# Kernel tuning notes

Hardware: AMD Instinct MI355X
Metric: run time of the kernel (lower is better)

The kernel has to match this reference:

```python
import jax, jax.numpy as jnp
import numpy as np

# dims: batch, seq, model dim, heads, head_k_dim, head_v_dim, conv size
B, S, D, H, DK, DV, K = 1, 2048, 1024, 8, 128, 128, 4
KD, VD = H * DK, H * DV  # key_dim, value_dim


def _silu(x):
    return x * jax.nn.sigmoid(x)


def _l2norm(x, eps=1e-6):
    return x * jax.lax.rsqrt(jnp.sum(x * x, -1, keepdims=True) + eps)


def _causal_conv_silu(x, w):
    # depthwise causal conv1d (ShortConvolution, activation='silu', no bias)
    # x: [b, s, d], w: [d, K]
    Kc = w.shape[1]
    xp = jnp.pad(x, ((0, 0), (Kc - 1, 0), (0, 0)))
    y = sum(xp[:, i:i + x.shape[1], :] * w[:, i] for i in range(Kc))
    return _silu(y)


def _rmsnorm(x, w, eps=1e-5):
    return x * jax.lax.rsqrt(jnp.mean(x * x, -1, keepdims=True) + eps) * w


def _kda(q, k, v, g, beta):
    # gated delta-rule linear attention (KDA), recurrent form == chunk_kda math
    # q,k,g: [B,S,H,DK]; v: [B,S,H,DV]; beta: [B,S,H]
    scale = DK ** -0.5
    qn = _l2norm(q) * scale  # use_qk_l2norm_in_kernel=True
    kn = _l2norm(k)

    def step(Sm, inp):
        q_t, k_t, v_t, g_t, b_t = inp  # [B,H,DK], [B,H,DK], [B,H,DV], [B,H,DK], [B,H]
        Sm = Sm * jnp.exp(g_t)[..., None]                    # per-key-channel decay
        v_new = (v_t - jnp.einsum('bhk,bhkv->bhv', k_t, Sm)) * b_t[..., None]
        Sm = Sm + k_t[..., None] * v_new[..., None, :]       # delta-rule update
        o_t = jnp.einsum('bhk,bhkv->bhv', q_t, Sm)
        return Sm, o_t

    xs = (jnp.swapaxes(qn, 0, 1), jnp.swapaxes(kn, 0, 1), jnp.swapaxes(v, 0, 1),
          jnp.swapaxes(g, 0, 1), jnp.swapaxes(beta, 0, 1))
    S0 = jnp.zeros((q.shape[0], H, DK, DV), jnp.float32)
    _, o = jax.lax.scan(step, S0, xs)
    return jnp.swapaxes(o, 0, 1)  # [B,S,H,DV]


def setup_inputs() -> dict:
    key = jax.random.key(0)
    ks = jax.random.split(key, 20)

    def w(k, shape, fan_in):
        return jax.random.normal(k, shape, jnp.float32) / np.sqrt(fan_in)

    return {
        'x': jax.random.normal(ks[0], (B, S, D), jnp.float32),
        've': jax.random.normal(ks[1], (B, S, D), jnp.float32),
        'sa_lambdas': jax.random.uniform(ks[2], (2,), jnp.float32),
        'Wq': w(ks[3], (KD, D), D), 'Wk': w(ks[4], (KD, D), D), 'Wv': w(ks[5], (VD, D), D),
        'Wo': w(ks[6], (D, VD), VD),
        'wq_conv': w(ks[7], (KD, K), K), 'wk_conv': w(ks[8], (KD, K), K), 'wv_conv': w(ks[9], (VD, K), K),
        'Wf1': w(ks[10], (DV, D), D), 'Wf2': w(ks[11], (KD, DV), DV),
        'Wb': w(ks[12], (H, D), D),
        'A_log': jnp.log(jax.random.uniform(ks[13], (H,), jnp.float32, 1.0, 16.0)),
        'dt_bias': jnp.zeros((KD,), jnp.float32),
        'Wg1': w(ks[14], (DV, D), D), 'Wg2': w(ks[15], (VD, DV), DV),
        'bg2': jnp.zeros((VD,), jnp.float32),
        'w_norm': jnp.ones((DV,), jnp.float32),
    }


def reference(x, ve, sa_lambdas, Wq, Wk, Wv, Wo, wq_conv, wk_conv, wv_conv,
              Wf1, Wf2, Wb, A_log, dt_bias, Wg1, Wg2, bg2, w_norm):
    b, s, _ = x.shape
    # q/k/v projections + short causal conv with silu
    q = _causal_conv_silu(x @ Wq.T, wq_conv)
    k = _causal_conv_silu(x @ Wk.T, wk_conv)
    v = _causal_conv_silu(x @ Wv.T, wv_conv)
    # fused_kda_gate: g = -exp(A_log) * softplus(f_proj(x) + dt_bias), per [H, DK]
    g = (x @ Wf1.T) @ Wf2.T
    g = jax.nn.softplus((g + dt_bias).astype(jnp.float32)).reshape(b, s, H, DK)
    g = -jnp.exp(A_log)[None, None, :, None] * g
    beta = jax.nn.sigmoid((x @ Wb.T).astype(jnp.float32))  # [b,s,H]
    q = q.reshape(b, s, H, DK)
    k = k.reshape(b, s, H, DK)
    v = v.reshape(b, s, H, DV)
    # mix v with value-embedding ve (3-D branch of _mix_v_with_ve)
    ve_v = _causal_conv_silu(ve @ Wv.T, wv_conv).reshape(b, s, H, DV)
    v = sa_lambdas[0] * v + sa_lambdas[1] * ve_v
    o = _kda(q, k, v, g, beta)  # [b,s,H,DV]
    # FusedRMSNormGated(activation='sigmoid'): rmsnorm(o)*w then gate
    g_out = ((x @ Wg1.T) @ Wg2.T + bg2).reshape(b, s, H, DV)
    o = _rmsnorm(o, w_norm) * jax.nn.sigmoid(g_out)
    return o.reshape(b, s, VD) @ Wo.T
```

## Files before the change

kernel.cpp:

```cpp
#include <hip/hip_runtime.h>
#include <math.h>
#include <stdint.h>

#define S_LEN 2048
#define DMODEL 1024
#define NH 8
#define DK_ 128
#define DV_ 128
#define KD_ 1024
#define KCONV 4
#define CW 32
#define NW2 64
#define PREB_STRIDE 17408
#define TKH_OFF 0
#define QHT_OFF 4096
#define KCT_OFF 8192
#define TV_OFF 12288
#define NN_OFF 16384
#define RS 164
#define GS 20

typedef short bf16x8 __attribute__((ext_vector_type(8)));
typedef float f32x4 __attribute__((ext_vector_type(4)));

__device__ __forceinline__ uint16_t f2bf(float f) {
  uint32_t u = __float_as_uint(f);
  u += 0x7FFF + ((u >> 16) & 1);
  return (uint16_t)(u >> 16);
}
__device__ __forceinline__ float bf2f(uint16_t u) {
  return __uint_as_float((uint32_t)u << 16);
}
__device__ __forceinline__ void glds16(const uint16_t* g, uint16_t* l) {
  __builtin_amdgcn_global_load_lds(
      (const __attribute__((address_space(1))) void*)g,
      (__attribute__((address_space(3))) void*)l, 16, 0, 0);
}
__device__ __forceinline__ float dot4(float4 a, float4 b) {
  return fmaf(a.w, b.w, fmaf(a.z, b.z, fmaf(a.y, b.y, a.x * b.x)));
}
__device__ __forceinline__ float4 f4add(float4 a, float4 b) {
  float4 r; r.x = a.x + b.x; r.y = a.y + b.y; r.z = a.z + b.z; r.w = a.w + b.w; return r;
}
__device__ __forceinline__ float4 f4sub(float4 a, float4 b) {
  float4 r; r.x = a.x - b.x; r.y = a.y - b.y; r.z = a.z - b.z; r.w = a.w - b.w; return r;
}
__device__ __forceinline__ float4 f4mul(float4 a, float4 b) {
  float4 r; r.x = a.x * b.x; r.y = a.y * b.y; r.z = a.z * b.z; r.w = a.w * b.w; return r;
}
__device__ __forceinline__ float4 f4s(float4 a, float s) {
  float4 r; r.x = a.x * s; r.y = a.y * s; r.z = a.z * s; r.w = a.w * s; return r;
}
__device__ __forceinline__ float4 f4expc(float4 a) {
  float4 r;
  r.x = expf(fminf(a.x, 0.f)); r.y = expf(fminf(a.y, 0.f));
  r.z = expf(fminf(a.z, 0.f)); r.w = expf(fminf(a.w, 0.f));
  return r;
}
__device__ __forceinline__ float4 f4exp(float4 a) {
  float4 r; r.x = expf(a.x); r.y = expf(a.y); r.z = expf(a.z); r.w = expf(a.w); return r;
}
__device__ __forceinline__ uint4 pack8(float4 a, float4 b) {
  uint4 r;
  r.x = (uint32_t)f2bf(a.x) | ((uint32_t)f2bf(a.y) << 16);
  r.y = (uint32_t)f2bf(a.z) | ((uint32_t)f2bf(a.w) << 16);
  r.z = (uint32_t)f2bf(b.x) | ((uint32_t)f2bf(b.y) << 16);
  r.w = (uint32_t)f2bf(b.z) | ((uint32_t)f2bf(b.w) << 16);
  return r;
}
__device__ __forceinline__ uint2 pack4(f32x4 a) {
  uint2 r;
  r.x = (uint32_t)f2bf(a[0]) | ((uint32_t)f2bf(a[1]) << 16);
  r.y = (uint32_t)f2bf(a[2]) | ((uint32_t)f2bf(a[3]) << 16);
  return r;
}
union U4B8 { uint4 u; bf16x8 b; };
__device__ __forceinline__ bf16x8 u2b(uint4 u) { U4B8 x; x.u = u; return x.b; }

#define DPPADD(x, ctrl) \
  x += __int_as_float(__builtin_amdgcn_update_dpp(0, __float_as_int(x), ctrl, 0xF, 0xF, true))

__device__ __forceinline__ void row8_sum2(float& a, float& b) {
  DPPADD(a, 0xB1); DPPADD(b, 0xB1);
  DPPADD(a, 0x4E); DPPADD(b, 0x4E);
  DPPADD(a, 0x141); DPPADD(b, 0x141);
}
__device__ __forceinline__ void row8_arr8x2(float* x, float* y) {
#pragma unroll
  for (int i = 0; i < 8; i++) { DPPADD(x[i], 0xB1); DPPADD(y[i], 0xB1); }
#pragma unroll
  for (int i = 0; i < 8; i++) { DPPADD(x[i], 0x4E); DPPADD(y[i], 0x4E); }
#pragma unroll
  for (int i = 0; i < 8; i++) { DPPADD(x[i], 0x141); DPPADD(y[i], 0x141); }
}

struct CastArgs {
  const float* s[8];
  uint16_t* d[8];
  int n[8];
};
__global__ __launch_bounds__(256) void cast_multi(CastArgs a, const float* __restrict__ Wb,
                                                  uint16_t* __restrict__ Wbp) {
  int i = blockIdx.y;
  if (i == 8) {
    for (int idx = blockIdx.x * 256 + threadIdx.x; idx < 128 * 1024; idx += 256 * 256) {
      int r = idx >> 10;
      Wbp[idx] = (r < 8) ? f2bf(Wb[idx]) : (uint16_t)0;
    }
    return;
  }
  const int step = gridDim.x * 256 * 8;
  for (int base = (blockIdx.x * 256 + threadIdx.x) * 8; base < a.n[i]; base += step) {
    const float4* sp = (const float4*)(a.s[i] + base);
    float4 x0 = sp[0], x1 = sp[1];
    *(uint4*)(a.d[i] + base) = pack8(x0, x1);
  }
}

__global__ __launch_bounds__(256) void gemm_wc(
    const float* __restrict__ A,
    const float* __restrict__ B,
    uint16_t* __restrict__ C) {
  __shared__ float As[16][68];
  __shared__ float Bs[16][68];
  const int tid = threadIdx.x;
  const int m0 = blockIdx.y * 64, n0 = blockIdx.x * 64;
  const int tx = tid & 15, ty = tid >> 4;
  const int lk = tid & 15, lr = tid >> 4;
  const int bc = tid & 63, bkr = tid >> 6;
  float acc[4][4] = {};
  for (int k0 = 0; k0 < 128; k0 += 16) {
#pragma unroll
    for (int i = 0; i < 4; i++) {
      As[lk][lr + 16 * i] = A[(size_t)(m0 + lr + 16 * i) * 128 + k0 + lk];
      Bs[bkr + 4 * i][bc] = B[(size_t)(k0 + bkr + 4 * i) * 1024 + n0 + bc];
    }
    __syncthreads();
#pragma unroll
    for (int kk = 0; kk < 16; kk++) {
      float4 a4 = *(const float4*)&As[kk][ty * 4];
      float4 b4 = *(const float4*)&Bs[kk][tx * 4];
      float av[4] = {a4.x, a4.y, a4.z, a4.w};
      float bv[4] = {b4.x, b4.y, b4.z, b4.w};
#pragma unroll
      for (int i = 0; i < 4; i++)
#pragma unroll
        for (int jx = 0; jx < 4; jx++) acc[i][jx] = fmaf(av[i], bv[jx], acc[i][jx]);
    }
    __syncthreads();
  }
#pragma unroll
  for (int i = 0; i < 4; i++)
#pragma unroll
    for (int jx = 0; jx < 4; jx++)
      C[(size_t)(m0 + ty * 4 + i) * 1024 + n0 + tx * 4 + jx] = f2bf(acc[i][jx]);
}

__device__ __forceinline__ void gemm_body(
    const uint16_t* __restrict__ A, const uint16_t* __restrict__ B, void* C,
    int N, int K, int outbf, int bx, int by, int tid,
    uint16_t* Asb, uint16_t* Bsb) {
  const int n0 = bx * 128;
  if (n0 >= N) return;
  const int w = tid >> 6, lane = tid & 63;
  const int m0 = by * 128;
  const int mw = (w & 1) * 64, nw = (w >> 1) * 64;
  const int c0 = tid, c1 = 256 + tid;
  const int r0 = c0 >> 2, cl0 = (c0 & 3) ^ ((r0 >> 2) & 3);
  const int r1 = c1 >> 2, cl1 = (c1 & 3) ^ ((r1 >> 2) & 3);
  const uint16_t* gA0 = A + (size_t)(m0 + r0) * K + cl0 * 8;
  const uint16_t* gA1 = A + (size_t)(m0 + r1) * K + cl1 * 8;
  const uint16_t* gB0 = B + (size_t)(n0 + r0) * K + cl0 * 8;
  const uint16_t* gB1 = B + (size_t)(n0 + r1) * K + cl1 * 8;
  uint16_t* lA0 = Asb + w * 512;
  uint16_t* lA1 = Asb + 2048 + w * 512;
  uint16_t* lB0 = Bsb + w * 512;
  uint16_t* lB1 = Bsb + 2048 + w * 512;

  const int l15 = lane & 15, q = lane >> 4;
  const int ccq = q ^ ((l15 >> 2) & 3);

  f32x4 acc[4][4] = {};
  for (int k0 = 0; k0 < K; k0 += 32) {
    glds16(gA0 + k0, lA0);
    glds16(gA1 + k0, lA1);
    glds16(gB0 + k0, lB0);
    glds16(gB1 + k0, lB1);
    __syncthreads();
    bf16x8 af[4], bfr[4];
#pragma unroll
    for (int i = 0; i < 4; i++)
      af[i] = *(const bf16x8*)&Asb[(mw + i * 16 + l15) * 32 + ccq * 8];
#pragma unroll
    for (int jx = 0; jx < 4; jx++)
      bfr[jx] = *(const bf16x8*)&Bsb[(nw + jx * 16 + l15) * 32 + ccq * 8];
#pragma unroll
    for (int i = 0; i < 4; i++)
#pragma unroll
      for (int jx = 0; jx < 4; jx++)
        acc[i][jx] = __builtin_amdgcn_mfma_f32_16x16x32_bf16(af[i], bfr[jx],
                                                             acc[i][jx], 0, 0, 0);
    __syncthreads();
  }
#pragma unroll
  for (int i = 0; i < 4; i++) {
#pragma unroll
    for (int jx = 0; jx < 4; jx++) {
      int n = n0 + nw + jx * 16 + l15;
#pragma unroll
      for (int r = 0; r < 4; r++) {
        int m = m0 + mw + i * 16 + q * 4 + r;
        if (outbf)
          ((uint16_t*)C)[(size_t)m * N + n] = f2bf(acc[i][jx][r]);
        else
          ((float*)C)[(size_t)m * N + n] = acc[i][jx][r];
      }
    }
  }
}

struct GJobs {
  const uint16_t* A[8];
  const uint16_t* B[8];
  void* C[8];
  int N[8];
  int outbf[8];
};
__global__ __launch_bounds__(256) void gemm_mfma(GJobs j, int K) {
  __shared__ uint16_t Asb[128 * 32];
  __shared__ uint16_t Bsb[128 * 32];
  const int z = blockIdx.z;
  gemm_body(j.A[z], j.B[z], j.C[z], j.N[z], K, j.outbf[z],
            blockIdx.x, blockIdx.y, threadIdx.x, Asb, Bsb);
}

__global__ __launch_bounds__(256) void conv_silu_mix(
    const uint16_t* __restrict__ qp, const uint16_t* __restrict__ kp,
    const uint16_t* __restrict__ vp, const uint16_t* __restrict__ vep,
    const float* __restrict__ wq, const float* __restrict__ wk,
    const float* __restrict__ wv, const float* __restrict__ lam,
    float* __restrict__ qc, float* __restrict__ kc, float* __restrict__ vmx) {
  int idx = blockIdx.x * 256 + threadIdx.x;
  if (idx >= S_LEN * KD_ / 8) return;
  int s = idx >> 7;
  int d0 = (idx & 127) * 8;
  const float lam0 = lam[0], lam1 = lam[1];

  union { uint4 u; ushort h[8]; } t;
  size_t base = (size_t)s * KD_ + d0;

  {
    float4 w4[8];
#pragma unroll
    for (int c = 0; c < 8; c++) w4[c] = *(const float4*)(wq + (size_t)d0 * 4 + c * 4);
    float acc[8] = {};
#pragma unroll
    for (int i = 0; i < KCONV; i++) {
      int ss = s - (KCONV - 1) + i;
      if (ss < 0) continue;
      t.u = *(const uint4*)(qp + (size_t)ss * KD_ + d0);
#pragma unroll
      for (int c = 0; c < 8; c++)
        acc[c] = fmaf(bf2f(t.h[c]), ((const float*)&w4[c])[i], acc[c]);
    }
    float out[8];
#pragma unroll
    for (int c = 0; c < 8; c++) out[c] = acc[c] / (1.f + expf(-acc[c]));
    *(float4*)(qc + base) = *(float4*)&out[0];
    *(float4*)(qc + base + 4) = *(float4*)&out[4];
  }
  {
    float4 w4[8];
#pragma unroll
    for (int c = 0; c < 8; c++) w4[c] = *(const float4*)(wk + (size_t)d0 * 4 + c * 4);
    float acc[8] = {};
#pragma unroll
    for (int i = 0; i < KCONV; i++) {
      int ss = s - (KCONV - 1) + i;
      if (ss < 0) continue;
      t.u = *(const uint4*)(kp + (size_t)ss * KD_ + d0);
#pragma unroll
      for (int c = 0; c < 8; c++)
        acc[c] = fmaf(bf2f(t.h[c]), ((const float*)&w4[c])[i], acc[c]);
    }
    float out[8];
#pragma unroll
    for (int c = 0; c < 8; c++) out[c] = acc[c] / (1.f + expf(-acc[c]));
    *(float4*)(kc + base) = *(float4*)&out[0];
    *(float4*)(kc + base + 4) = *(float4*)&out[4];
  }
  {
    float4 w4[8];
#pragma unroll
    for (int c = 0; c < 8; c++) w4[c] = *(const float4*)(wv + (size_t)d0 * 4 + c * 4);
    float av[8] = {}, ae[8] = {};
#pragma unroll
    for (int i = 0; i < KCONV; i++) {
      int ss = s - (KCONV - 1) + i;
      if (ss < 0) continue;
      size_t off = (size_t)ss * KD_ + d0;
      t.u = *(const uint4*)(vp + off);
#pragma unroll
      for (int c = 0; c < 8; c++)
        av[c] = fmaf(bf2f(t.h[c]), ((const float*)&w4[c])[i], av[c]);
      t.u = *(const uint4*)(vep + off);
#pragma unroll
      for (int c = 0; c < 8; c++)
        ae[c] = fmaf(bf2f(t.h[c]), ((const float*)&w4[c])[i], ae[c]);
    }
    float out[8];
#pragma unroll
    for (int c = 0; c < 8; c++) {
      float sv = av[c] / (1.f + expf(-av[c]));
      float se = ae[c] / (1.f + expf(-ae[c]));
      out[c] = lam0 * sv + lam1 * se;
    }
    *(float4*)(vmx + base) = *(float4*)&out[0];
    *(float4*)(vmx + base + 4) = *(float4*)&out[4];
  }
}

__global__ __launch_bounds__(256) void kda_pre(
    const float* __restrict__ qc, const float* __restrict__ kc,
    const float* __restrict__ graw, const float* __restrict__ vm,
    const float* __restrict__ bpre, const float* __restrict__ dt_bias,
    const float* __restrict__ A_log, uint16_t* __restrict__ preB,
    float* __restrict__ preF) {
  __shared__ float kls[32 * RS];
  __shared__ float Gls[32 * RS];
  __shared__ float Mcm[32 * 36];
  __shared__ float bls[32];
  const int w = blockIdx.x >> 3, h = blockIdx.x & 7;
  const int tid = threadIdx.x;
  const int t = tid >> 3, kq = tid & 7;
  const int wv = tid >> 6;
  const size_t gb = (size_t)blockIdx.x * PREB_STRIDE;
  const size_t gf = (size_t)blockIdx.x * 128;

  size_t roff = (size_t)(w * CW + t) * KD_ + h * DK_ + kq * 16;
  float4 kv[4], qv[4], gv[4], dtb[4];
#pragma unroll
  for (int i = 0; i < 4; i++) {
    kv[i] = *(const float4*)(kc + roff + i * 4);
    qv[i] = *(const float4*)(qc + roff + i * 4);
    gv[i] = *(const float4*)(graw + roff + i * 4);
    dtb[i] = *(const float4*)(dt_bias + h * DK_ + kq * 16 + i * 4);
  }
  const float Ahead = expf(A_log[h]);
  if (tid < 32) {
    float b = bpre[(size_t)(w * CW + tid) * 128 + h];
    bls[tid] = 1.f / (1.f + expf(-b));
  }
  float src[32];
  if (tid >= 128) {
    int c2 = tid - 128;
#pragma unroll
    for (int t2 = 0; t2 < 32; t2++)
      src[t2] = vm[(size_t)(w * CW + t2) * KD_ + h * DV_ + c2];
  }
#pragma unroll
  for (int i = 0; i < 4; i++) {
    float vsp[4];
    float xin[4] = {gv[i].x + dtb[i].x, gv[i].y + dtb[i].y,
                    gv[i].z + dtb[i].z, gv[i].w + dtb[i].w};
#pragma unroll
    for (int e = 0; e < 4; e++)
      vsp[e] = (xin[e] > 20.f) ? xin[e] : log1pf(expf(xin[e]));
    gv[i].x = -Ahead * vsp[0]; gv[i].y = -Ahead * vsp[1];
    gv[i].z = -Ahead * vsp[2]; gv[i].w = -Ahead * vsp[3];
  }
  float sk = 0.f, sq = 0.f;
#pragma unroll
  for (int i = 0; i < 4; i++) {
    sk += dot4(kv[i], kv[i]);
    sq += dot4(qv[i], qv[i]);
  }
  row8_sum2(sk, sq);
  float rkn = rsqrtf(sk + 1e-6f);
  float rqn = rsqrtf(sq + 1e-6f) * 0.08838834764831845f;
#pragma unroll
  for (int i = 0; i < 4; i++) {
    kv[i] = f4s(kv[i], rkn);
    qv[i] = f4s(qv[i], rqn);
    *(float4*)&kls[t * RS + kq * GS + i * 4] = kv[i];
    *(float4*)&Gls[t * RS + kq * GS + i * 4] = gv[i];
  }
  __syncthreads();
  float4 Ga[4] = {};
#pragma unroll
  for (int jb = 0; jb < 4; jb++) {
    if (jb <= wv) {
#pragma unroll
      for (int jj = 0; jj < 8; jj++) {
        int j = jb * 8 + jj;
        bool inc = (jb < wv) || (j <= t);
#pragma unroll
        for (int i = 0; i < 4; i++) {
          float4 gj = *(const float4*)&Gls[j * RS + kq * GS + i * 4];
          if (inc) Ga[i] = f4add(Ga[i], gj);
        }
      }
    }
  }
  __syncthreads();
  float4 khr[4];
  float4 Pa[4];
#pragma unroll
  for (int i = 0; i < 4; i++) {
    *(float4*)&Gls[t * RS + kq * GS + i * 4] = Ga[i];
    Pa[i] = f4exp(Ga[i]);
    khr[i] = f4mul(kv[i], Pa[i]);
  }
  {
    float4 q0 = f4mul(qv[0], Pa[0]), q1 = f4mul(qv[1], Pa[1]);
    float4 q2 = f4mul(qv[2], Pa[2]), q3 = f4mul(qv[3], Pa[3]);
    *(uint4*)(preB + gb + QHT_OFF + t * 128 + kq * 16) = pack8(q0, q1);
    *(uint4*)(preB + gb + QHT_OFF + t * 128 + kq * 16 + 8) = pack8(q2, q3);
  }
  if (t == 31) {
#pragma unroll
    for (int i = 0; i < 4; i++)
      *(float4*)(preF + gf + kq * 16 + i * 4) = Pa[i];
  }
  __syncthreads();
#pragma unroll
  for (int i = 0; i < 4; i++) {
    float4 Gfi = *(const float4*)&Gls[31 * RS + kq * GS + i * 4];
    float4 ea = f4expc(f4sub(Gfi, Ga[i]));
    float4 kc4 = f4mul(kv[i], ea);
    float kk[4] = {kc4.x, kc4.y, kc4.z, kc4.w};
#pragma unroll
    for (int e = 0; e < 4; e++)
      preB[gb + KCT_OFF + (kq * 16 + i * 4 + e) * 32 + t] = f2bf(kk[e]);
  }
#pragma unroll
  for (int jb = 0; jb < 4; jb++) {
    if (jb <= wv) {
      float mp8[8], np8[8];
#pragma unroll
      for (int jj = 0; jj < 8; jj++) {
        int j = jb * 8 + jj;
        float m = 0.f, n = 0.f;
#pragma unroll
        for (int i = 0; i < 4; i++) {
          float4 kj = *(const float4*)&kls[j * RS + kq * GS + i * 4];
          float4 Gj = *(const float4*)&Gls[j * RS + kq * GS + i * 4];
          float4 e = f4expc(f4sub(Ga[i], Gj));
          float4 p = f4mul(kj, e);
          m += dot4(kv[i], p);
          n += dot4(qv[i], p);
        }
        mp8[jj] = (j < t) ? m : 0.f;
        np8[jj] = (j <= t) ? n : 0.f;
      }
      row8_arr8x2(mp8, np8);
#pragma unroll
      for (int jj = 0; jj < 8; jj++) {
        if (kq == jj) {
          int j = jb * 8 + jj;
          Mcm[j * 36 + t] = bls[t] * mp8[jj];
          preB[gb + NN_OFF + t * 32 + j] = f2bf(np8[jj]);
        }
      }
    } else {
      preB[gb + NN_OFF + t * 32 + jb * 8 + kq] = 0;
    }
  }
  float bl[32];
#pragma unroll
  for (int i = 0; i < 8; i++) {
    float4 b4 = *(const float4*)&bls[i * 4];
    bl[i * 4 + 0] = b4.x; bl[i * 4 + 1] = b4.y;
    bl[i * 4 + 2] = b4.z; bl[i * 4 + 3] = b4.w;
  }
  __syncthreads();
#pragma unroll
  for (int i = 0; i < 4; i++)
    *(float4*)&kls[t * RS + kq * GS + i * 4] = khr[i];
  __syncthreads();
  if (tid < 128) {
#pragma unroll
    for (int t2 = 0; t2 < 32; t2++)
      src[t2] = kls[t2 * RS + (tid >> 4) * GS + (tid & 15)];
  }
  const int c = tid;
  float acc[32];
#pragma unroll
  for (int i = 0; i < 32; i++) acc[i] = 0.f;
#pragma unroll
  for (int t2 = 0; t2 < 32; t2++) {
    float val = fmaf(bl[t2], src[t2], -acc[t2]);
    if (c < 128)
      preB[gb + TKH_OFF + t2 * 128 + c] = f2bf(val);
    else
      preB[gb + TV_OFF + t2 * 128 + (c - 128)] = f2bf(val);
#pragma unroll
    for (int t3 = t2 + 1; t3 < 32; t3++)
      acc[t3] = fmaf(Mcm[t2 * 36 + t3], val, acc[t3]);
  }
}

__global__ __launch_bounds__(256) void kda_scan_g2(
    const uint16_t* __restrict__ preB, const float* __restrict__ preF,
    float* __restrict__ o, const uint16_t* __restrict__ g1b,
    const uint16_t* __restrict__ Wg2b, float* __restrict__ g2raw) {
  __shared__ uint16_t tkh[2][32 * 136];
  __shared__ uint16_t qht[2][32 * 136];
  __shared__ uint16_t sbf[16 * 136];
  __shared__ uint16_t vbf[16 * 40];
  __shared__ uint16_t Asb[128 * 32];
  __shared__ uint16_t Bsb[128 * 32];
  const int bid = blockIdx.x;
  const int tid = threadIdx.x;

  if (bid >= 64) {
    int b2 = bid - 64;
    gemm_body(g1b, Wg2b, g2raw, 1024, 128, 0, b2 & 7, b2 >> 3, tid, Asb, Bsb);
    return;
  }

  const int h = bid & 7, cg = bid >> 3;
  const int wv = tid >> 6, lane = tid & 63;
  const int q = lane >> 4, l15 = lane & 15;

  auto stage = [&](int w, int buf) {
    size_t gbs = (size_t)(w * 8 + h) * PREB_STRIDE;
    const uint4* gt = (const uint4*)(preB + gbs + TKH_OFF);
    const uint4* gq = (const uint4*)(preB + gbs + QHT_OFF);
    int row = lane >> 1, half = lane & 1;
    uint4 a[8], b[8];
#pragma unroll
    for (int i = 0; i < 8; i++) {
      a[i] = gt[lane * 8 + i];
      b[i] = gq[lane * 8 + i];
    }
#pragma unroll
    for (int i = 0; i < 8; i++) {
      *(uint4*)&tkh[buf][row * 136 + half * 64 + i * 8] = a[i];
      *(uint4*)&qht[buf][row * 136 + half * 64 + i * 8] = b[i];
    }
  };

  f32x4 s[8] = {};

  if (wv == 1) stage(0, 0);
  __syncthreads();

  for (int w = 0; w < NW2; w++) {
    if (wv == 1) {
      if (w + 1 < NW2) stage(w + 1, (w + 1) & 1);
    } else if (wv == 0) {
      const int buf = w & 1;
      const size_t gbs = (size_t)(w * 8 + h) * PREB_STRIDE;
      uint4 kct[8], nrg[2];
      float4 pb[8];
      float tvv[2][4];
#pragma unroll
      for (int ki = 0; ki < 8; ki++)
        kct[ki] = *(const uint4*)(preB + gbs + KCT_OFF + (16 * ki + l15) * 32 + q * 8);
#pragma unroll
      for (int tt = 0; tt < 2; tt++)
        nrg[tt] = *(const uint4*)(preB + gbs + NN_OFF + (tt * 16 + l15) * 32 + q * 8);
#pragma unroll
      for (int ki = 0; ki < 8; ki++)
        pb[ki] = *(const float4*)(preF + (size_t)(w * 8 + h) * 128 + 16 * ki + q * 4);
#pragma unroll
      for (int tt = 0; tt < 2; tt++)
#pragma unroll
        for (int r = 0; r < 4; r++)
          tvv[tt][r] = bf2f(preB[gbs + TV_OFF + (tt * 16 + q * 4 + r) * 128 + cg * 16 + l15]);
#pragma unroll
      for (int ki = 0; ki < 8; ki++)
        *(uint2*)&sbf[l15 * 136 + 16 * ki + q * 4] = pack4(s[ki]);
      f32x4 aat[2] = {}, bbt[2] = {};
      __builtin_amdgcn_s_setprio(1);
#pragma unroll
      for (int kc = 0; kc < 4; kc++) {
        bf16x8 bS = *(const bf16x8*)&sbf[l15 * 136 + kc * 32 + q * 8];
#pragma unroll
        for (int tt = 0; tt < 2; tt++) {
          bf16x8 aT = *(const bf16x8*)&tkh[buf][(tt * 16 + l15) * 136 + kc * 32 + q * 8];
          bf16x8 aQ = *(const bf16x8*)&qht[buf][(tt * 16 + l15) * 136 + kc * 32 + q * 8];
          aat[tt] = __builtin_amdgcn_mfma_f32_16x16x32_bf16(aT, bS, aat[tt], 0, 0, 0);
          bbt[tt] = __builtin_amdgcn_mfma_f32_16x16x32_bf16(aQ, bS, bbt[tt], 0, 0, 0);
        }
      }
      __builtin_amdgcn_s_setprio(0);
#pragma unroll
      for (int tt = 0; tt < 2; tt++) {
        f32x4 vn;
#pragma unroll
        for (int r = 0; r < 4; r++) vn[r] = tvv[tt][r] - aat[tt][r];
        *(uint2*)&vbf[l15 * 40 + tt * 16 + q * 4] = pack4(vn);
      }
      bf16x8 bV = *(const bf16x8*)&vbf[l15 * 40 + q * 8];
      __builtin_amdgcn_s_setprio(1);
#pragma unroll
      for (int tt = 0; tt < 2; tt++) {
        f32x4 ot = __builtin_amdgcn_mfma_f32_16x16x32_bf16(u2b(nrg[tt]), bV,
                                                           bbt[tt], 0, 0, 0);
#pragma unroll
        for (int r = 0; r < 4; r++)
          o[(size_t)(w * CW + tt * 16 + q * 4 + r) * KD_ + h * DK_ + cg * 16 + l15] = ot[r];
      }
#pragma unroll
      for (int ki = 0; ki < 8; ki++) {
#pragma unroll
        for (int r = 0; r < 4; r++) s[ki][r] *= pb[ki][r];
        s[ki] = __builtin_amdgcn_mfma_f32_16x16x32_bf16(u2b(kct[ki]), bV, s[ki], 0, 0, 0);
      }
      __builtin_amdgcn_s_setprio(0);
    }
    __syncthreads();
  }
}

__global__ __launch_bounds__(64) void gated_rmsnorm(
    const float* __restrict__ o, const float* __restrict__ g2raw,
    const float* __restrict__ bg2, const float* __restrict__ wn,
    uint16_t* __restrict__ ob) {
  size_t base = (size_t)blockIdx.x * DV_;
  int t = threadIdx.x;
  float a = o[base + t], b = o[base + t + 64];
  float ss = a * a + b * b;
#pragma unroll
  for (int off = 32; off > 0; off >>= 1) ss += __shfl_xor(ss, off);
  float r = rsqrtf(ss * (1.f / 128.f) + 1e-5f);
  int c0 = (int)((base + t) & 1023), c1 = (int)((base + t + 64) & 1023);
  float ga = 1.f / (1.f + expf(-(g2raw[base + t] + bg2[c0])));
  float gb = 1.f / (1.f + expf(-(g2raw[base + t + 64] + bg2[c1])));
  ob[base + t] = f2bf(a * r * wn[t] * ga);
  ob[base + t + 64] = f2bf(b * r * wn[t + 64] * gb);
}

extern "C" void kernel_launch(void* const* d_in, const int* in_sizes, int n_in,
                              void* d_out, int out_size, void* d_ws, size_t ws_size,
                              hipStream_t stream) {
  const float* x = (const float*)d_in[0];
  const float* ve = (const float*)d_in[1];
  const float* lam = (const float*)d_in[2];
  const float* Wq = (const float*)d_in[3];
  const float* Wk = (const float*)d_in[4];
  const float* Wv = (const float*)d_in[5];
  const float* Wo = (const float*)d_in[6];
  const float* wq_conv = (const float*)d_in[7];
  const float* wk_conv = (const float*)d_in[8];
  const float* wv_conv = (const float*)d_in[9];
  const float* Wf1 = (const float*)d_in[10];
  const float* Wf2 = (const float*)d_in[11];
  const float* Wb = (const float*)d_in[12];
  const float* A_log = (const float*)d_in[13];
  const float* dt_bias = (const float*)d_in[14];
  const float* Wg1 = (const float*)d_in[15];
  const float* Wg2 = (const float*)d_in[16];
  const float* bg2 = (const float*)d_in[17];
  const float* w_norm = (const float*)d_in[18];
  float* out = (float*)d_out;

  float* ws = (float*)d_ws;
  const size_t SZ = (size_t)S_LEN * KD_;
  uint16_t* qpb = (uint16_t*)ws;
  uint16_t* kpb = (uint16_t*)(ws + SZ / 2);
  uint16_t* vpb = (uint16_t*)(ws + SZ);
  uint16_t* vepb = (uint16_t*)(ws + 3 * SZ / 2);
  float* q_c = ws + 2 * SZ;
  float* k_c = ws + 3 * SZ;
  float* v_mix = ws + 4 * SZ;
  float* graw = ws + 5 * SZ;
  float* o_buf = graw;
  float* g2raw = k_c;
  uint16_t* bws = (uint16_t*)(ws + 6 * SZ);
  uint16_t* xb = bws;
  uint16_t* veb = xb + SZ;
  uint16_t* Wqb = veb + SZ;
  uint16_t* Wkb = Wqb + (size_t)KD_ * DMODEL;
  uint16_t* Wvb = Wkb + (size_t)KD_ * DMODEL;
  uint16_t* Wob = Wvb + (size_t)KD_ * DMODEL;
  uint16_t* Wg1b = Wob + (size_t)DMODEL * KD_;
  uint16_t* Wg2b = Wg1b + (size_t)DV_ * DMODEL;
  uint16_t* Wcb = Wg2b + (size_t)KD_ * DV_;
  uint16_t* Wbp = Wcb + (size_t)KD_ * DMODEL;
  uint16_t* g1b = Wbp + (size_t)128 * 1024;
  uint16_t* ob = g1b + (size_t)S_LEN * DV_;
  float* bpre2 = ws + 18 * (size_t)1024 * 1024;
  float* preF = ws + (size_t)20 * 1024 * 1024;
  uint16_t* preB = (uint16_t*)(ws + (size_t)20 * 1024 * 1024 + 65536 + 64);

  dim3 blk(256);

  CastArgs ca;
  ca.s[0] = x;   ca.d[0] = xb;   ca.n[0] = S_LEN * DMODEL;
  ca.s[1] = ve;  ca.d[1] = veb;  ca.n[1] = S_LEN * DMODEL;
  ca.s[2] = Wq;  ca.d[2] = Wqb;  ca.n[2] = KD_ * DMODEL;
  ca.s[3] = Wk;  ca.d[3] = Wkb;  ca.n[3] = KD_ * DMODEL;
  ca.s[4] = Wv;  ca.d[4] = Wvb;  ca.n[4] = KD_ * DMODEL;
  ca.s[5] = Wo;  ca.d[5] = Wob;  ca.n[5] = DMODEL * KD_;
  ca.s[6] = Wg1; ca.d[6] = Wg1b; ca.n[6] = DV_ * DMODEL;
  ca.s[7] = Wg2; ca.d[7] = Wg2b; ca.n[7] = KD_ * DV_;
  cast_multi<<<dim3(256, 9), blk, 0, stream>>>(ca, Wb, Wbp);

  gemm_wc<<<dim3(16, 16), blk, 0, stream>>>(Wf2, Wf1, Wcb);

  GJobs jq;
  jq.A[0] = xb;  jq.B[0] = Wqb;  jq.C[0] = qpb;   jq.N[0] = KD_; jq.outbf[0] = 1;
  jq.A[1] = xb;  jq.B[1] = Wkb;  jq.C[1] = kpb;   jq.N[1] = KD_; jq.outbf[1] = 1;
  jq.A[2] = xb;  jq.B[2] = Wvb;  jq.C[2] = vpb;   jq.N[2] = KD_; jq.outbf[2] = 1;
  jq.A[3] = veb; jq.B[3] = Wvb;  jq.C[3] = vepb;  jq.N[3] = KD_; jq.outbf[3] = 1;
  jq.A[4] = xb;  jq.B[4] = Wg1b; jq.C[4] = g1b;   jq.N[4] = DV_; jq.outbf[4] = 1;
  jq.A[5] = xb;  jq.B[5] = Wcb;  jq.C[5] = graw;  jq.N[5] = KD_; jq.outbf[5] = 0;
  jq.A[6] = xb;  jq.B[6] = Wbp;  jq.C[6] = bpre2; jq.N[6] = 128; jq.outbf[6] = 0;
  gemm_mfma<<<dim3(8, 16, 7), blk, 0, stream>>>(jq, DMODEL);

  int conv_blocks = (S_LEN * KD_ / 8 + 255) / 256;
  conv_silu_mix<<<conv_blocks, blk, 0, stream>>>(qpb, kpb, vpb, vepb,
                                                 wq_conv, wk_conv, wv_conv, lam,
                                                 q_c, k_c, v_mix);

  kda_pre<<<dim3(NW2 * 8), blk, 0, stream>>>(q_c, k_c, graw, v_mix, bpre2,
                                             dt_bias, A_log, preB, preF);

  kda_scan_g2<<<dim3(192), blk, 0, stream>>>(preB, preF, o_buf, g1b, Wg2b, g2raw);

  gated_rmsnorm<<<dim3(S_LEN * NH), dim3(64), 0, stream>>>(o_buf, g2raw, bg2,
                                                           w_norm, ob);

  GJobs jo;
  jo.A[0] = ob; jo.B[0] = Wob; jo.C[0] = out; jo.N[0] = DMODEL; jo.outbf[0] = 0;
  gemm_mfma<<<dim3(8, 16, 1), blk, 0, stream>>>(jo, KD_);
}
```

Measured before the change: 383.3 us.

## Fold Wf2·Wf1 weight GEMM into cast kernel and drop setprio hints

Moves the small fp32 GEMM that forms the combined Wf2·Wf1 weight into the multi-cast kernel as an extra grid row (blockIdx.y==9), so one launch does both jobs and the GEMM runs alongside the casts. This removes a kernel launch and the serialization between the two preprocessing kernels. It also removes the s_setprio wave-priority hints around the MFMA sections of the recurrent KDA kernel, which changes how waves are scheduled in the hot loop. The fused kernel now always allocates static LDS for the GEMM tiles, which may lower occupancy for the cast blocks.

After: 383.1 us. Within noise of the previous version (-0.0%).

```diff
diff --git a/kernel.cpp b/kernel.cpp
--- a/kernel.cpp
+++ b/kernel.cpp
@@ -99,9 +99,48 @@
   uint16_t* d[8];
   int n[8];
 };
-__global__ __launch_bounds__(256) void cast_multi(CastArgs a, const float* __restrict__ Wb,
-                                                  uint16_t* __restrict__ Wbp) {
+__global__ __launch_bounds__(256) void cast_multi(
+    CastArgs a, const float* __restrict__ Wb, uint16_t* __restrict__ Wbp,
+    const float* __restrict__ Wf2,
+    const float* __restrict__ Wf1,
+    uint16_t* __restrict__ Wcb) {
+  __shared__ float As[16][68];
+  __shared__ float Bs[16][68];
   int i = blockIdx.y;
+  if (i == 9) {
+    const int tid = threadIdx.x;
+    const int m0 = (blockIdx.x >> 4) * 64, n0 = (blockIdx.x & 15) * 64;
+    const int tx = tid & 15, ty = tid >> 4;
+    const int lk = tid & 15, lr = tid >> 4;
+    const int bc = tid & 63, bkr = tid >> 6;
+    float acc[4][4] = {};
+    for (int k0 = 0; k0 < 128; k0 += 16) {
+#pragma unroll
+      for (int ii = 0; ii < 4; ii++) {
+        As[lk][lr + 16 * ii] = Wf2[(size_t)(m0 + lr + 16 * ii) * 128 + k0 + lk];
+        Bs[bkr + 4 * ii][bc] = Wf1[(size_t)(k0 + bkr + 4 * ii) * 1024 + n0 + bc];
+      }
+      __syncthreads();
+#pragma unroll
+      for (int kk = 0; kk < 16; kk++) {
+        float4 a4 = *(const float4*)&As[kk][ty * 4];
+        float4 b4 = *(const float4*)&Bs[kk][tx * 4];
+        float av[4] = {a4.x, a4.y, a4.z, a4.w};
+        float bv[4] = {b4.x, b4.y, b4.z, b4.w};
+#pragma unroll
+        for (int ii = 0; ii < 4; ii++)
+#pragma unroll
+          for (int jx = 0; jx < 4; jx++) acc[ii][jx] = fmaf(av[ii], bv[jx], acc[ii][jx]);
+      }
+      __syncthreads();
+    }
+#pragma unroll
+    for (int ii = 0; ii < 4; ii++)
+#pragma unroll
+      for (int jx = 0; jx < 4; jx++)
+        Wcb[(size_t)(m0 + ty * 4 + ii) * 1024 + n0 + tx * 4 + jx] = f2bf(acc[ii][jx]);
+    return;
+  }
   if (i == 8) {
     for (int idx = blockIdx.x * 256 + threadIdx.x; idx < 128 * 1024; idx += 256 * 256) {
       int r = idx >> 10;
@@ -115,45 +154,6 @@
     float4 x0 = sp[0], x1 = sp[1];
     *(uint4*)(a.d[i] + base) = pack8(x0, x1);
   }
-}
-
-__global__ __launch_bounds__(256) void gemm_wc(
-    const float* __restrict__ A,
-    const float* __restrict__ B,
-    uint16_t* __restrict__ C) {
-  __shared__ float As[16][68];
-  __shared__ float Bs[16][68];
-  const int tid = threadIdx.x;
-  const int m0 = blockIdx.y * 64, n0 = blockIdx.x * 64;
-  const int tx = tid & 15, ty = tid >> 4;
-  const int lk = tid & 15, lr = tid >> 4;
-  const int bc = tid & 63, bkr = tid >> 6;
-  float acc[4][4] = {};
-  for (int k0 = 0; k0 < 128; k0 += 16) {
-#pragma unroll
-    for (int i = 0; i < 4; i++) {
-      As[lk][lr + 16 * i] = A[(size_t)(m0 + lr + 16 * i) * 128 + k0 + lk];
-      Bs[bkr + 4 * i][bc] = B[(size_t)(k0 + bkr + 4 * i) * 1024 + n0 + bc];
-    }
-    __syncthreads();
-#pragma unroll
-    for (int kk = 0; kk < 16; kk++) {
-      float4 a4 = *(const float4*)&As[kk][ty * 4];
-      float4 b4 = *(const float4*)&Bs[kk][tx * 4];
-      float av[4] = {a4.x, a4.y, a4.z, a4.w};
-      float bv[4] = {b4.x, b4.y, b4.z, b4.w};
-#pragma unroll
-      for (int i = 0; i < 4; i++)
-#pragma unroll
-        for (int jx = 0; jx < 4; jx++) acc[i][jx] = fmaf(av[i], bv[jx], acc[i][jx]);
-    }
-    __syncthreads();
-  }
-#pragma unroll
-  for (int i = 0; i < 4; i++)
-#pragma unroll
-    for (int jx = 0; jx < 4; jx++)
-      C[(size_t)(m0 + ty * 4 + i) * 1024 + n0 + tx * 4 + jx] = f2bf(acc[i][jx]);
 }
 
 __device__ __forceinline__ void gemm_body(
@@ -573,7 +573,6 @@
       for (int ki = 0; ki < 8; ki++)
         *(uint2*)&sbf[l15 * 136 + 16 * ki + q * 4] = pack4(s[ki]);
       f32x4 aat[2] = {}, bbt[2] = {};
-      __builtin_amdgcn_s_setprio(1);
 #pragma unroll
       for (int kc = 0; kc < 4; kc++) {
         bf16x8 bS = *(const bf16x8*)&sbf[l15 * 136 + kc * 32 + q * 8];
@@ -585,7 +584,6 @@
           bbt[tt] = __builtin_amdgcn_mfma_f32_16x16x32_bf16(aQ, bS, bbt[tt], 0, 0, 0);
         }
       }
-      __builtin_amdgcn_s_setprio(0);
 #pragma unroll
       for (int tt = 0; tt < 2; tt++) {
         f32x4 vn;
@@ -594,7 +592,6 @@
         *(uint2*)&vbf[l15 * 40 + tt * 16 + q * 4] = pack4(vn);
       }
       bf16x8 bV = *(const bf16x8*)&vbf[l15 * 40 + q * 8];
-      __builtin_amdgcn_s_setprio(1);
 #pragma unroll
       for (int tt = 0; tt < 2; tt++) {
         f32x4 ot = __builtin_amdgcn_mfma_f32_16x16x32_bf16(u2b(nrg[tt]), bV,
@@ -609,7 +606,6 @@
         for (int r = 0; r < 4; r++) s[ki][r] *= pb[ki][r];
         s[ki] = __builtin_amdgcn_mfma_f32_16x16x32_bf16(u2b(kct[ki]), bV, s[ki], 0, 0, 0);
       }
-      __builtin_amdgcn_s_setprio(0);
     }
     __syncthreads();
   }
@@ -697,9 +693,7 @@
   ca.s[5] = Wo;  ca.d[5] = Wob;  ca.n[5] = DMODEL * KD_;
   ca.s[6] = Wg1; ca.d[6] = Wg1b; ca.n[6] = DV_ * DMODEL;
   ca.s[7] = Wg2; ca.d[7] = Wg2b; ca.n[7] = KD_ * DV_;
-  cast_multi<<<dim3(256, 9), blk, 0, stream>>>(ca, Wb, Wbp);
-
-  gemm_wc<<<dim3(16, 16), blk, 0, stream>>>(Wf2, Wf1, Wcb);
+  cast_multi<<<dim3(256, 10), blk, 0, stream>>>(ca, Wb, Wbp, Wf2, Wf1, Wcb);
 
   GJobs jq;
   jq.A[0] = xb;  jq.B[0] = Wqb;  jq.C[0] = qpb;   jq.N[0] = KD_; jq.outbf[0] = 1;
```
